# Optimization experiments

Hardware: AMD Instinct MI355X
Metric: run time of the kernel (lower is better)

The kernel has to match this reference:

```python
import jax, jax.numpy as jnp
from jax import lax
import numpy as np

EPS = 1e-08
BETA_VAL = 0.9
B_VAL = 1.0
SIGMA_VAL = 10.0

@jax.custom_vjp
def spike_fn(mthr, sigma):
    # Heaviside forward; SuperSpike surrogate gradient in backward
    return (mthr > 0).astype(mthr.dtype)

def _spike_fwd(mthr, sigma):
    return (mthr > 0).astype(mthr.dtype), (mthr, sigma)

def _spike_bwd(res, g):
    mthr, sigma = res
    grad = g / (sigma * jnp.abs(mthr) + 1.0) ** 2
    return grad, jnp.zeros_like(sigma)

spike_fn.defvjp(_spike_fwd, _spike_bwd)


def setup_inputs() -> dict:
    key = jax.random.key(0)
    kx, kw, kv = jax.random.split(key, 3)
    B, T, I, O = 128, 100, 1024, 1024
    x = jax.random.normal(kx, (B, T, I), dtype=jnp.float32)
    w = (jax.random.normal(kw, (I, O), dtype=jnp.float32)
         * np.float32(np.sqrt(1.0 / I)))  # mean 0, std w_init_std*sqrt(1/I)
    v = (jax.random.normal(kv, (O, O), dtype=jnp.float32)
         * np.float32(np.sqrt(1.0 / O)))
    beta = jnp.full((1,), BETA_VAL, dtype=jnp.float32)   # one_per_layer
    b = jnp.full((O,), B_VAL, dtype=jnp.float32)
    sigma = jnp.full((O,), SIGMA_VAL, dtype=jnp.float32)  # surrogate_sigma_mode='all'
    return {"x": x, "w": w, "v": v, "beta": beta, "b": b, "sigma": sigma}


def reference(x, w, v, beta, b, sigma):
    B, T, I = x.shape
    O = w.shape[1]
    h = jnp.einsum('bti,io->bto', x, w)            # [B,T,O]
    d = jnp.einsum('ai,ao->io', w, w)              # lateral term w^T w, [O,O]
    norm = (w ** 2).sum(0)                         # [O]
    inv_norm = 1.0 / (norm + EPS)

    mem0 = jnp.zeros((B, O), dtype=x.dtype)
    spk0 = jnp.zeros((B, O), dtype=x.dtype)

    def step(carry, h_t):
        mem, spk = carry
        rst = spk @ d                              # lateral reset [B,O]
        inp = h_t + spk @ v                        # recurrent input
        # Leaky neuron, soft reset
        mem = (mem - rst) * beta + inp * (1.0 - beta)
        mthr = mem * inv_norm - b
        spk = spike_fn(mthr, sigma)
        return (mem, spk), spk

    h_t_first = jnp.swapaxes(h, 0, 1)              # [T,B,O]
    _, spk_seq = lax.scan(step, (mem0, spk0), h_t_first)
    spk_rec = jnp.swapaxes(spk_seq, 0, 1)          # [B,T,O]

    loss = 0.5 * (spk_rec ** 2).mean()             # Regularization 'squared'
    spk_spread_loss = spk_rec.sum(axis=(0, 2)).max() / (B * O)  # 'max'
    return spk_rec, loss, spk_spread_loss
```

## Files before the change

### kernel.cpp

```cpp
#include <hip/hip_runtime.h>
#include <cstdint>
#include <cstddef>

#define I_DIM 1024
#define O_DIM 1024
#define B_DIM 128
#define T_DIM 100
#define PANEL 32768
#define QSTep 512

typedef __attribute__((ext_vector_type(8))) __bf16 bf16x8;
typedef __attribute__((ext_vector_type(16))) float f32x16;

__device__ __forceinline__ void wg_barrier_lgkm() {
  __asm__ volatile("" ::: "memory");
  __builtin_amdgcn_s_waitcnt(0xC07F);
  __builtin_amdgcn_s_barrier();
  __asm__ volatile("" ::: "memory");
}

__device__ __forceinline__ unsigned short bf16rn(float x) {
  unsigned u = __float_as_uint(x);
  unsigned r = u + 0x7FFFu + ((u >> 16) & 1u);
  return (unsigned short)(r >> 16);
}
__device__ __forceinline__ void split2(float x, unsigned short& h,
                                       unsigned short& l) {
  h = bf16rn(x);
  float hf = __uint_as_float(((unsigned)h) << 16);
  l = bf16rn(x - hf);
}

__global__ __launch_bounds__(256) void prep_kernel(
    const float* __restrict__ w, const float* __restrict__ x,
    unsigned short* __restrict__ wTth, unsigned short* __restrict__ wTtl,
    unsigned short* __restrict__ xth, unsigned short* __restrict__ xtl,
    double* __restrict__ normpart) {
  __shared__ float tile[64][65];
  __shared__ double red[4][64];
  const int id = blockIdx.x;
  const int tid = threadIdx.x;
  if (id < 256) {
    const int a0 = (id >> 4) * 64, o0 = (id & 15) * 64;
    const int tr = tid >> 4, tc4 = (tid & 15) * 4;
#pragma unroll
    for (int rr = 0; rr < 64; rr += 16) {
      float4 v = *(const float4*)&w[(size_t)(a0 + tr + rr) * O_DIM + o0 + tc4];
      tile[tr + rr][tc4 + 0] = v.x;
      tile[tr + rr][tc4 + 1] = v.y;
      tile[tr + rr][tc4 + 2] = v.z;
      tile[tr + rr][tc4 + 3] = v.w;
    }
    __syncthreads();
    {
      const int ol = tid & 63, seg = tid >> 6;
      double s = 0.0;
#pragma unroll
      for (int i = 0; i < 16; ++i) {
        double v = (double)tile[seg * 16 + i][ol];
        s += v * v;
      }
      red[seg][ol] = s;
    }
    const int q = (a0 >> 4) + (tc4 >> 4);
    const int kh = (tc4 >> 3) & 1;
    const int inner = tc4 & 7;
#pragma unroll
    for (int rr = 0; rr < 64; rr += 16) {
      int o = o0 + tr + rr;
      unsigned short hh[4], ll[4];
#pragma unroll
      for (int j = 0; j < 4; ++j) split2(tile[tc4 + j][tr + rr], hh[j], ll[j]);
      int l = (o & 31) + 32 * kh;
      size_t base = ((size_t)(o >> 5) * PANEL) + (size_t)q * QSTep +
                    (size_t)l * 8 + inner;
      *(ushort4*)&wTth[base] = make_ushort4(hh[0], hh[1], hh[2], hh[3]);
      *(ushort4*)&wTtl[base] = make_ushort4(ll[0], ll[1], ll[2], ll[3]);
    }
    __syncthreads();
    if (tid < 64)
      normpart[(size_t)(a0 >> 6) * O_DIM + o0 + tid] =
          red[0][tid] + red[1][tid] + red[2][tid] + red[3][tid];
  } else {
    const int p = id - 256;
    const int wq = tid >> 6, lane = tid & 63;
    const int row = lane & 31, kh = lane >> 5;
    const float* src = x + (size_t)(p * 32 + row) * I_DIM + kh * 8;
#pragma unroll 4
    for (int i = 0; i < 16; ++i) {
      const int q = i * 4 + wq;
      const float* s = src + q * 16;
      float4 v0 = *(const float4*)(s);
      float4 v1 = *(const float4*)(s + 4);
      unsigned short h[8], l[8];
      split2(v0.x, h[0], l[0]);
      split2(v0.y, h[1], l[1]);
      split2(v0.z, h[2], l[2]);
      split2(v0.w, h[3], l[3]);
      split2(v1.x, h[4], l[4]);
      split2(v1.y, h[5], l[5]);
      split2(v1.z, h[6], l[6]);
      split2(v1.w, h[7], l[7]);
      size_t base = ((size_t)p * PANEL) + (size_t)q * QSTep + (size_t)lane * 8;
      *(ushort4*)&xth[base] = make_ushort4(h[0], h[1], h[2], h[3]);
      *(ushort4*)&xth[base + 4] = make_ushort4(h[4], h[5], h[6], h[7]);
      *(ushort4*)&xtl[base] = make_ushort4(l[0], l[1], l[2], l[3]);
      *(ushort4*)&xtl[base + 4] = make_ushort4(l[4], l[5], l[6], l[7]);
    }
  }
}

__global__ __launch_bounds__(256) void gemm_fused(
    const unsigned short* __restrict__ xth,
    const unsigned short* __restrict__ xtl,
    const unsigned short* __restrict__ wTth,
    const unsigned short* __restrict__ wTtl, const float* __restrict__ v,
    const float* __restrict__ beta_p, float* __restrict__ h,
    float* __restrict__ M) {
  const int tid = threadIdx.x;
  const int wv = tid >> 6, lane = tid & 63;
  const int lm = lane & 31, lkh = lane >> 5;
  if (blockIdx.y < 100) {
    const int lin = blockIdx.y * 16 + blockIdx.x;
    const int slin = (lin & 7) * 200 + (lin >> 3);
    const int row0 = (slin >> 4) * 128, col0 = (slin & 15) * 64;
    const int wm = wv >> 1, wn = wv & 1;
    f32x16 acc[2];
#pragma unroll
    for (int a = 0; a < 2; ++a)
#pragma unroll
      for (int e = 0; e < 16; ++e) acc[a][e] = 0.f;
    const unsigned short *pah[2], *pal[2], *pbh, *pbl;
#pragma unroll
    for (int mt = 0; mt < 2; ++mt) {
      size_t offA =
          ((size_t)((row0 >> 5) + wm * 2 + mt) * PANEL) + (size_t)lane * 8;
      pah[mt] = xth + offA;
      pal[mt] = xtl + offA;
    }
    {
      size_t offB = ((size_t)((col0 >> 5) + wn) * PANEL) + (size_t)lane * 8;
      pbh = wTth + offB;
      pbl = wTtl + offB;
    }
    bf16x8 fah[2][2], fal[2][2], fbh[2], fbl[2];
#pragma unroll
    for (int mt = 0; mt < 2; ++mt) {
      fah[0][mt] = *(const bf16x8*)(pah[mt]);
      fal[0][mt] = *(const bf16x8*)(pal[mt]);
    }
    fbh[0] = *(const bf16x8*)(pbh);
    fbl[0] = *(const bf16x8*)(pbl);
#pragma unroll 2
    for (int q = 0; q < 64; ++q) {
      const int cb = q & 1;
      if (q < 63) {
        size_t d = (size_t)(q + 1) * QSTep;
#pragma unroll
        for (int mt = 0; mt < 2; ++mt) {
          fah[cb ^ 1][mt] = *(const bf16x8*)(pah[mt] + d);
          fal[cb ^ 1][mt] = *(const bf16x8*)(pal[mt] + d);
        }
        fbh[cb ^ 1] = *(const bf16x8*)(pbh + d);
        fbl[cb ^ 1] = *(const bf16x8*)(pbl + d);
      }
#pragma unroll
      for (int mt = 0; mt < 2; ++mt)
        acc[mt] = __builtin_amdgcn_mfma_f32_32x32x16_bf16(fah[cb][mt], fbh[cb],
                                                          acc[mt], 0, 0, 0);
#pragma unroll
      for (int mt = 0; mt < 2; ++mt)
        acc[mt] = __builtin_amdgcn_mfma_f32_32x32x16_bf16(fah[cb][mt], fbl[cb],
                                                          acc[mt], 0, 0, 0);
#pragma unroll
      for (int mt = 0; mt < 2; ++mt)
        acc[mt] = __builtin_amdgcn_mfma_f32_32x32x16_bf16(fal[cb][mt], fbh[cb],
                                                          acc[mt], 0, 0, 0);
    }
    const int col = col0 + wn * 32 + lm;
#pragma unroll
    for (int mt = 0; mt < 2; ++mt)
#pragma unroll
      for (int r = 0; r < 16; ++r) {
        int row = row0 + wm * 64 + mt * 32 + (r & 3) + 8 * (r >> 2) + 4 * lkh;
        h[(size_t)row * O_DIM + col] = acc[mt][r];
      }
  } else {
    const int i0 = (blockIdx.y - 100) * 64, o0 = blockIdx.x * 64;
    const int wm = wv >> 1, wn = wv & 1;
    f32x16 acc;
#pragma unroll
    for (int e = 0; e < 16; ++e) acc[e] = 0.f;
    const size_t offA = ((size_t)((i0 >> 5) + wm) * PANEL) + (size_t)lane * 8;
    const size_t offB = ((size_t)((o0 >> 5) + wn) * PANEL) + (size_t)lane * 8;
    bf16x8 ah[2], al[2], bh[2], bl[2];
    ah[0] = *(const bf16x8*)(wTth + offA);
    al[0] = *(const bf16x8*)(wTtl + offA);
    bh[0] = *(const bf16x8*)(wTth + offB);
    bl[0] = *(const bf16x8*)(wTtl + offB);
#pragma unroll 2
    for (int q = 0; q < 64; ++q) {
      const int cb = q & 1;
      if (q < 63) {
        size_t d = (size_t)(q + 1) * QSTep;
        ah[cb ^ 1] = *(const bf16x8*)(wTth + offA + d);
        al[cb ^ 1] = *(const bf16x8*)(wTtl + offA + d);
        bh[cb ^ 1] = *(const bf16x8*)(wTth + offB + d);
        bl[cb ^ 1] = *(const bf16x8*)(wTtl + offB + d);
      }
      acc =
          __builtin_amdgcn_mfma_f32_32x32x16_bf16(ah[cb], bh[cb], acc, 0, 0, 0);
      acc =
          __builtin_amdgcn_mfma_f32_32x32x16_bf16(ah[cb], bl[cb], acc, 0, 0, 0);
      acc =
          __builtin_amdgcn_mfma_f32_32x32x16_bf16(al[cb], bh[cb], acc, 0, 0, 0);
    }
    const float beta = beta_p[0];
    const float ombeta = 1.0f - beta;
    const int col = o0 + wn * 32 + lm;
#pragma unroll
    for (int r = 0; r < 16; ++r) {
      int row = i0 + wm * 32 + (r & 3) + 8 * (r >> 2) + 4 * lkh;
      M[(size_t)row * O_DIM + col] =
          ombeta * v[(size_t)row * O_DIM + col] - beta * acc[r];
    }
  }
}

__global__ __launch_bounds__(512) void scan_kernel(
    const float* __restrict__ h, const float* __restrict__ M,
    const double* __restrict__ normpart, const float* __restrict__ bvec,
    const float* __restrict__ beta_p, float* __restrict__ out,
    int* __restrict__ wgcnt) {
  __shared__ unsigned short wlist[2][8][128];
  __shared__ int wcnt[2][8];
  const int b = blockIdx.x, tid = threadIdx.x;
  const int wv = tid >> 6;
  const int o0 = tid * 2;
  const double beta = (double)beta_p[0];
  const double ombeta = 1.0 - beta;
  double mem[2] = {0.0, 0.0};
  double inv[2], bth[2];
  {
    double s0 = 0.0, s1 = 0.0;
#pragma unroll
    for (int g = 0; g < 16; ++g) {
      double2 np = *(const double2*)&normpart[(size_t)g * O_DIM + o0];
      s0 += np.x;
      s1 += np.y;
    }
    inv[0] = 1.0 / (s0 + 1e-8);
    inv[1] = 1.0 / (s1 + 1e-8);
    float2 bv = *(const float2*)&bvec[o0];
    bth[0] = (double)bv.x;
    bth[1] = (double)bv.y;
  }
  if (tid < 16) wcnt[tid >> 3][tid & 7] = 0;
  __syncthreads();
  const float* hb = h + (size_t)b * T_DIM * O_DIM;
  float* ob = out + (size_t)b * T_DIM * O_DIM;
  float2 hv0 = *(const float2*)&hb[o0];
  float2 hv1 = *(const float2*)&hb[O_DIM + o0];
  for (int t = 0; t < T_DIM; ++t) {
    const int p = t & 1, np = p ^ 1;
    float2 hv2 = make_float2(0.f, 0.f);
    if (t + 2 < T_DIM) hv2 = *(const float2*)&hb[(size_t)(t + 2) * O_DIM + o0];
    double l0[2] = {0.0, 0.0}, l1[2] = {0.0, 0.0};
    double l2[2] = {0.0, 0.0}, l3[2] = {0.0, 0.0};
    int ks = 0;
#pragma unroll
    for (int w = 0; w < 8; ++w) ks += wcnt[p][w];
    if (ks) {
#pragma unroll
      for (int w = 0; w < 8; ++w) {
        const int kw = wcnt[p][w];
        const unsigned short* wl = wlist[p][w];
        int n = 0;
        for (; n + 4 <= kw; n += 4) {
          float2 m0 = *(const float2*)&M[(size_t)wl[n] * O_DIM + o0];
          float2 m1 = *(const float2*)&M[(size_t)wl[n + 1] * O_DIM + o0];
          float2 m2 = *(const float2*)&M[(size_t)wl[n + 2] * O_DIM + o0];
          float2 m3 = *(const float2*)&M[(size_t)wl[n + 3] * O_DIM + o0];
          l0[0] += (double)m0.x;
          l0[1] += (double)m0.y;
          l1[0] += (double)m1.x;
          l1[1] += (double)m1.y;
          l2[0] += (double)m2.x;
          l2[1] += (double)m2.y;
          l3[0] += (double)m3.x;
          l3[1] += (double)m3.y;
        }
        for (; n < kw; ++n) {
          float2 mr = *(const float2*)&M[(size_t)wl[n] * O_DIM + o0];
          l0[0] += (double)mr.x;
          l0[1] += (double)mr.y;
        }
      }
    }
    double lat0 = (l0[0] + l1[0]) + (l2[0] + l3[0]);
    double lat1 = (l0[1] + l1[1]) + (l2[1] + l3[1]);
    mem[0] = mem[0] * beta + (double)hv0.x * ombeta + lat0;
    mem[1] = mem[1] * beta + (double)hv0.y * ombeta + lat1;
    bool s0 = (mem[0] * inv[0] - bth[0]) > 0.0;
    bool s1 = (mem[1] * inv[1] - bth[1]) > 0.0;
    *(float2*)&ob[(size_t)t * O_DIM + o0] =
        make_float2(s0 ? 1.0f : 0.0f, s1 ? 1.0f : 0.0f);
    unsigned cur = 0;
    {
      unsigned long long mask = __ballot(s0);
      if (s0) {
        unsigned below = __builtin_amdgcn_mbcnt_lo((unsigned)mask, 0);
        below = __builtin_amdgcn_mbcnt_hi((unsigned)(mask >> 32), below);
        wlist[np][wv][cur + below] = (unsigned short)o0;
      }
      cur += (unsigned)__popcll(mask);
    }
    {
      unsigned long long mask = __ballot(s1);
      if (s1) {
        unsigned below = __builtin_amdgcn_mbcnt_lo((unsigned)mask, 0);
        below = __builtin_amdgcn_mbcnt_hi((unsigned)(mask >> 32), below);
        wlist[np][wv][cur + below] = (unsigned short)(o0 + 1);
      }
      cur += (unsigned)__popcll(mask);
    }
    hv0 = hv1;
    hv1 = hv2;
    if ((tid & 63) == 0) wcnt[np][wv] = (int)cur;
    wg_barrier_lgkm();
    if (tid == 0)
      wgcnt[b * T_DIM + t] = wcnt[np][0] + wcnt[np][1] + wcnt[np][2] +
                             wcnt[np][3] + wcnt[np][4] + wcnt[np][5] +
                             wcnt[np][6] + wcnt[np][7];
  }
}

__global__ void finalize_kernel(const int* __restrict__ wgcnt,
                                float* __restrict__ out) {
  __shared__ int sums[128];
  const int t = threadIdx.x;
  int s = 0;
  if (t < T_DIM) {
    for (int b = 0; b < B_DIM; ++b) s += wgcnt[b * T_DIM + t];
  }
  sums[t] = s;
  __syncthreads();
  if (t == 0) {
    long long total = 0;
    int mx = 0;
    for (int i = 0; i < T_DIM; ++i) {
      total += sums[i];
      if (sums[i] > mx) mx = sums[i];
    }
    const double N = (double)B_DIM * T_DIM * O_DIM;
    out[(size_t)B_DIM * T_DIM * O_DIM] = (float)(0.5 * (double)total / N);
    out[(size_t)B_DIM * T_DIM * O_DIM + 1] =
        (float)((double)mx / (double)(B_DIM * O_DIM));
  }
}

extern "C" void kernel_launch(void* const* d_in, const int* in_sizes, int n_in,
                              void* d_out, int out_size, void* d_ws,
                              size_t ws_size, hipStream_t stream) {
  const float* x = (const float*)d_in[0];
  const float* w = (const float*)d_in[1];
  const float* v = (const float*)d_in[2];
  const float* beta = (const float*)d_in[3];
  const float* b = (const float*)d_in[4];
  float* out = (float*)d_out;

  char* ws = (char*)d_ws;
  const size_t OFF_M = 0;
  const size_t OFF_H = 4194304;
  const size_t OFF_WTH = 56623104;
  const size_t OFF_WTL = 58720256;
  const size_t OFF_NP = 60817408;
  const size_t OFF_XTH = 60948992;
  const size_t OFF_XTL = 87163392;
  float* M = (float*)(ws + OFF_M);
  float* h = (float*)(ws + OFF_H);
  unsigned short* wTth = (unsigned short*)(ws + OFF_WTH);
  unsigned short* wTtl = (unsigned short*)(ws + OFF_WTL);
  double* normpart = (double*)(ws + OFF_NP);
  unsigned short* xth = (unsigned short*)(ws + OFF_XTH);
  unsigned short* xtl = (unsigned short*)(ws + OFF_XTL);
  int* wgcnt = (int*)(ws + OFF_XTH);

  hipLaunchKernelGGL(prep_kernel, dim3(656), dim3(256), 0, stream, w, x, wTth,
                     wTtl, xth, xtl, normpart);
  hipLaunchKernelGGL(gemm_fused, dim3(16, 116), dim3(256), 0, stream, xth, xtl,
                     wTth, wTtl, v, beta, h, M);
  hipLaunchKernelGGL(scan_kernel, dim3(128), dim3(512), 0, stream, h, M,
                     normpart, b, beta, out, wgcnt);
  hipLaunchKernelGGL(finalize_kernel, dim3(1), dim3(128), 0, stream, wgcnt,
                     out);
}
```

Measured before the change: 300.0 us.

## Stage GEMM operand panels through shared memory to remove duplicate global loads

In the h-projection GEMM branch, each wave previously loaded its own A and B fragments directly from global memory, so waves sharing row or column panels issued redundant loads. The block now loads each panel slice once cooperatively into LDS, with one register prefetch of the next step, then reads the MFMA fragments from LDS. This cuts global traffic per block but adds two __syncthreads per K step and LDS round trips. With only 3 MFMA pairs per step, the barriers may dominate.

```diff
diff --git a/kernel.cpp b/kernel.cpp
--- a/kernel.cpp
+++ b/kernel.cpp
@@ -117,6 +117,7 @@
     const unsigned short* __restrict__ wTtl, const float* __restrict__ v,
     const float* __restrict__ beta_p, float* __restrict__ h,
     float* __restrict__ M) {
+  __shared__ __align__(16) unsigned short sbuf[6144];
   const int tid = threadIdx.x;
   const int wv = tid >> 6, lane = tid & 63;
   const int lm = lane & 31, lkh = lane >> 5;
@@ -130,52 +131,64 @@
     for (int a = 0; a < 2; ++a)
 #pragma unroll
       for (int e = 0; e < 16; ++e) acc[a][e] = 0.f;
-    const unsigned short *pah[2], *pal[2], *pbh, *pbl;
-#pragma unroll
-    for (int mt = 0; mt < 2; ++mt) {
-      size_t offA =
-          ((size_t)((row0 >> 5) + wm * 2 + mt) * PANEL) + (size_t)lane * 8;
-      pah[mt] = xth + offA;
-      pal[mt] = xtl + offA;
-    }
+    const unsigned short* gs0;
+    const unsigned short* gs1;
+    const unsigned short* gs2;
+    int lo0, lo1, lo2;
     {
-      size_t offB = ((size_t)((col0 >> 5) + wn) * PANEL) + (size_t)lane * 8;
-      pbh = wTth + offB;
-      pbl = wTtl + offB;
-    }
-    bf16x8 fah[2][2], fal[2][2], fbh[2], fbl[2];
-#pragma unroll
-    for (int mt = 0; mt < 2; ++mt) {
-      fah[0][mt] = *(const bf16x8*)(pah[mt]);
-      fal[0][mt] = *(const bf16x8*)(pal[mt]);
-    }
-    fbh[0] = *(const bf16x8*)(pbh);
-    fbl[0] = *(const bf16x8*)(pbl);
-#pragma unroll 2
+      const int p = tid >> 6, w16 = (tid & 63) * 8;
+      gs0 = xth + ((size_t)((row0 >> 5) + p) * PANEL) + w16;
+      gs1 = xtl + ((size_t)((row0 >> 5) + p) * PANEL) + w16;
+      lo0 = tid * 8;
+      lo1 = 2048 + tid * 8;
+      if (tid < 128) {
+        const int pp = tid >> 6, ww = (tid & 63) * 8;
+        gs2 = wTth + ((size_t)((col0 >> 5) + pp) * PANEL) + ww;
+        lo2 = 4096 + tid * 8;
+      } else {
+        const int tb = tid - 128;
+        const int pp = tb >> 6, ww = (tb & 63) * 8;
+        gs2 = wTtl + ((size_t)((col0 >> 5) + pp) * PANEL) + ww;
+        lo2 = 5120 + tb * 8;
+      }
+    }
+    uint4 r0 = *(const uint4*)(gs0);
+    uint4 r1 = *(const uint4*)(gs1);
+    uint4 r2 = *(const uint4*)(gs2);
+    const int fa0 = (wm * 2 + 0) * 512 + lane * 8;
+    const int fa1 = (wm * 2 + 1) * 512 + lane * 8;
+    const int fb = 4096 + wn * 512 + lane * 8;
     for (int q = 0; q < 64; ++q) {
-      const int cb = q & 1;
+      *(uint4*)&sbuf[lo0] = r0;
+      *(uint4*)&sbuf[lo1] = r1;
+      *(uint4*)&sbuf[lo2] = r2;
+      __syncthreads();
       if (q < 63) {
         size_t d = (size_t)(q + 1) * QSTep;
-#pragma unroll
-        for (int mt = 0; mt < 2; ++mt) {
-          fah[cb ^ 1][mt] = *(const bf16x8*)(pah[mt] + d);
-          fal[cb ^ 1][mt] = *(const bf16x8*)(pal[mt] + d);
-        }
-        fbh[cb ^ 1] = *(const bf16x8*)(pbh + d);
-        fbl[cb ^ 1] = *(const bf16x8*)(pbl + d);
-      }
+        r0 = *(const uint4*)(gs0 + d);
+        r1 = *(const uint4*)(gs1 + d);
+        r2 = *(const uint4*)(gs2 + d);
+      }
+      bf16x8 fah[2], fal[2], fbh, fbl;
+      fah[0] = *(const bf16x8*)&sbuf[fa0];
+      fah[1] = *(const bf16x8*)&sbuf[fa1];
+      fal[0] = *(const bf16x8*)&sbuf[2048 + fa0];
+      fal[1] = *(const bf16x8*)&sbuf[2048 + fa1];
+      fbh = *(const bf16x8*)&sbuf[fb];
+      fbl = *(const bf16x8*)&sbuf[1024 + fb];
 #pragma unroll
       for (int mt = 0; mt < 2; ++mt)
-        acc[mt] = __builtin_amdgcn_mfma_f32_32x32x16_bf16(fah[cb][mt], fbh[cb],
-                                                          acc[mt], 0, 0, 0);
+        acc[mt] = __builtin_amdgcn_mfma_f32_32x32x16_bf16(fah[mt], fbh, acc[mt],
+                                                          0, 0, 0);
 #pragma unroll
       for (int mt = 0; mt < 2; ++mt)
-        acc[mt] = __builtin_amdgcn_mfma_f32_32x32x16_bf16(fah[cb][mt], fbl[cb],
-                                                          acc[mt], 0, 0, 0);
+        acc[mt] = __builtin_amdgcn_mfma_f32_32x32x16_bf16(fah[mt], fbl, acc[mt],
+                                                          0, 0, 0);
 #pragma unroll
       for (int mt = 0; mt < 2; ++mt)
-        acc[mt] = __builtin_amdgcn_mfma_f32_32x32x16_bf16(fal[cb][mt], fbh[cb],
-                                                          acc[mt], 0, 0, 0);
+        acc[mt] = __builtin_amdgcn_mfma_f32_32x32x16_bf16(fal[mt], fbh, acc[mt],
+                                                          0, 0, 0);
+      __syncthreads();
     }
     const int col = col0 + wn * 32 + lm;
 #pragma unroll
```

After: 297.1 us. About the same (-1.0%).
